# Optimization experiments

Hardware: AMD Instinct MI355X
Metric: run time of the kernel (lower is better)

## Reference

```python
import jax, jax.numpy as jnp
import numpy as np
from jax import lax

EMB, HDIM, OBS_LEN = 64, 64, 8
BATCH, NSCENES, SCENE = 32768, 4096, 8
SEQ_LEN = 12


def setup_inputs() -> dict:
    key = jax.random.key(0)
    ks = jax.random.split(key, 16)
    obs_traj = jax.random.normal(ks[0], (OBS_LEN, BATCH, 2), jnp.float32)
    last_pos = jax.random.normal(ks[1], (BATCH, 2), jnp.float32)
    last_pos_rel = jax.random.normal(ks[2], (BATCH, 2), jnp.float32)
    starts = jnp.arange(NSCENES, dtype=jnp.int32) * SCENE
    seq_start_end = jnp.stack([starts, starts + SCENE], axis=1)  # (NSCENES, 2)
    # spatial_embedding: Linear(2, EMB)
    W_se = jax.random.normal(ks[3], (EMB, 2), jnp.float32) * 0.5
    b_se = jax.random.normal(ks[4], (EMB,), jnp.float32) * 0.1
    # weight-normed convs: w = g * v / ||v||_(in,k) per out-channel, bias init zero
    def conv_params(k, cout, cin, ksz):
        ka, kb = jax.random.split(k)
        std = np.sqrt(4.0 / (ksz * cin))
        v = jax.random.normal(ka, (cout, cin, ksz), jnp.float32) * std
        g = jax.random.uniform(kb, (cout,), jnp.float32, 0.5, 1.5)
        b = jnp.zeros((cout,), jnp.float32)
        return v, g, b
    v1, g1, b1 = conv_params(ks[5], HDIM, EMB, 3)
    v2, g2, b2 = conv_params(ks[6], HDIM // 2, HDIM, 3)
    v3, g3, b3 = conv_params(ks[7], HDIM // 2, HDIM // 2, 3)
    # hidden2pos: Linear(2*HDIM, 2)
    W_hp = jax.random.normal(ks[8], (2, 2 * HDIM), jnp.float32) * 0.05
    b_hp = jax.random.normal(ks[9], (2,), jnp.float32) * 0.05
    return {"obs_traj": obs_traj, "last_pos": last_pos, "last_pos_rel": last_pos_rel,
            "W_se": W_se, "b_se": b_se,
            "v1": v1, "g1": g1, "b1": b1,
            "v2": v2, "g2": g2, "b2": b2,
            "v3": v3, "g3": g3, "b3": b3,
            "W_hp": W_hp, "b_hp": b_hp,
            "seq_start_end": seq_start_end, "seq_len": SEQ_LEN}


def _wn_conv_relu(x, v, g, b):
    # weight-norm: w[o] = g[o] * v[o] / ||v[o]||  (norm over in-channels and kernel)
    norm = jnp.sqrt(jnp.sum(v * v, axis=(1, 2)))
    w = v * (g / norm)[:, None, None]
    y = lax.conv_general_dilated(x, w, (1,), 'VALID',
                                 dimension_numbers=('NCH', 'OIH', 'NCH'))
    return jax.nn.relu(y + b[None, :, None])


def reference(obs_traj, last_pos, last_pos_rel,
              W_se, b_se, v1, g1, b1, v2, g2, b2, v3, g3, b3, W_hp, b_hp,
              seq_start_end, seq_len):
    batch = last_pos.shape[0]
    nseg = seq_start_end.shape[0]
    h_dim = v1.shape[0]
    # scene id for each pedestrian (segments are contiguous [start,end) ranges)
    seg = jnp.searchsorted(seq_start_end[:, 0], jnp.arange(batch), side='right') - 1
    # obs_traj embedding -> (batch, EMB, OBS_LEN)
    emb = obs_traj @ W_se.T + b_se            # (T, B, EMB)
    obs_emb0 = jnp.transpose(emb, (1, 2, 0))  # (B, EMB, T)

    def step(carry, _):
        obs_emb, lp = carry
        s = _wn_conv_relu(obs_emb, v1, g1, b1)   # (B, H, T-2)
        s = _wn_conv_relu(s, v2, g2, b2)         # (B, H/2, T-4)
        s = _wn_conv_relu(s, v3, g3, b3)         # (B, H/2, T-6)
        s = s.reshape(batch, h_dim)              # (H/2)*(T-6) == H
        mx = jax.ops.segment_max(s, seg, num_segments=nseg)  # ragged per-scene max
        st = jnp.concatenate([s, mx[seg]], axis=1)           # (B, 2H)
        rel = st @ W_hp.T + b_hp                 # (B, 2)
        lp = rel + lp
        dec = rel @ W_se.T + b_se                # (B, EMB)
        obs_emb = jnp.concatenate([obs_emb[:, :, 1:], dec[:, :, None]], axis=2)
        return (obs_emb, lp), rel

    _, rels = lax.scan(step, (obs_emb0, last_pos), None, length=seq_len)
    return rels  # (seq_len, batch, 2)
```

## Files before the change

### kernel.cpp

```cpp
#include <hip/hip_runtime.h>

#define BATCH 32768
#define SEQLEN 12
#define PEDS 16
#define NBLK (BATCH/PEDS)

typedef short short8 __attribute__((ext_vector_type(8)));
typedef float f32x4 __attribute__((ext_vector_type(4)));

static __device__ __forceinline__ unsigned short f2bf(float x) {
    unsigned u = __float_as_uint(x);
    return (unsigned short)((u + 0x7FFFu + ((u >> 16) & 1u)) >> 16);
}
static __device__ __forceinline__ float bf2f(unsigned short h) {
    return __uint_as_float(((unsigned)h) << 16);
}
static __device__ __forceinline__ int mod6(int h) {
    h = (h >= 12) ? h - 12 : h;
    return (h >= 6) ? h - 6 : h;
}

__global__ __launch_bounds__(256, 3)
void enc_main(const float* __restrict__ obs,
              const float* __restrict__ Wse, const float* __restrict__ bse,
              const float* __restrict__ v1, const float* __restrict__ g1, const float* __restrict__ b1,
              const float* __restrict__ v2, const float* __restrict__ g2, const float* __restrict__ b2,
              const float* __restrict__ v3, const float* __restrict__ g3, const float* __restrict__ b3,
              const float* __restrict__ Whp, const float* __restrict__ bhp,
              float* __restrict__ out)
{
    __shared__ __align__(16) float pos[8][PEDS][2];
    __shared__ __align__(16) unsigned short s1h[6][PEDS][72], s1l[6][PEDS][72];
    __shared__ __align__(16) unsigned short s2h[4][PEDS][40], s2l[4][PEDS][40];
    __shared__ __align__(16) float sff[2][PEDS][68];
    __shared__ __align__(16) float mxs[2][2][68];

    float* wse_s = &sff[0][0][0];
    float* bse_s = wse_s + 128;
    float* sc_s  = wse_s + 192;
    float* a1c   = wse_s + 320;
    float* b1c   = wse_s + 512;
    float* c1c   = wse_s + 704;

    const int tid  = threadIdx.x;
    const int wv   = tid >> 6;
    const int lane = tid & 63;
    const int n    = lane & 15;
    const int kg   = lane >> 4;

    if (tid < 128) wse_s[tid] = Wse[tid];
    else if (tid < 192) bse_s[tid-128] = bse[tid-128];
    if (tid < 64) {
        const float* v = v1 + tid*192; float s = 0.f;
        for (int j = 0; j < 192; j++) s += v[j]*v[j];
        sc_s[tid] = g1[tid] / sqrtf(s);
    } else if (tid < 96) {
        const float* v = v2 + (tid-64)*192; float s = 0.f;
        for (int j = 0; j < 192; j++) s += v[j]*v[j];
        sc_s[tid] = g2[tid-64] / sqrtf(s);
    } else if (tid < 128) {
        const float* v = v3 + (tid-96)*96; float s = 0.f;
        for (int j = 0; j < 96; j++) s += v[j]*v[j];
        sc_s[tid] = g3[tid-96] / sqrtf(s);
    }
    __syncthreads();

    {
        int tau = tid >> 5, p = (tid >> 1) & 15, c = tid & 1;
        pos[tau][p][c] = obs[(tau*BATCH + blockIdx.x*PEDS + p)*2 + c];
    }
    if (tid < 192) {
        int oc = tid & 63, tap = tid >> 6;
        const float* vr = v1 + oc*192 + tap;
        float dA = 0.f, dB = 0.f, dC = 0.f;
        #pragma unroll 8
        for (int ic = 0; ic < 64; ++ic) {
            float w = vr[ic*3];
            dA = fmaf(w, wse_s[ic*2],   dA);
            dB = fmaf(w, wse_s[ic*2+1], dB);
            dC = fmaf(w, bse_s[ic],     dC);
        }
        a1c[tap*64+oc] = dA; b1c[tap*64+oc] = dB; c1c[tap*64+oc] = dC;
    }
    __syncthreads();

    const int c_p = tid >> 4, c_oc0 = (tid & 15) * 4;
    float cA[3][4], cB[3][4], K1[4];
    #pragma unroll
    for (int j = 0; j < 4; ++j) {
        int oc = c_oc0 + j; float s = sc_s[oc];
        float cs = 0.f;
        #pragma unroll
        for (int tap = 0; tap < 3; ++tap) {
            cA[tap][j] = s * a1c[tap*64+oc];
            cB[tap][j] = s * b1c[tap*64+oc];
            cs += c1c[tap*64+oc];
        }
        K1[j] = fmaf(s, cs, b1[oc]);
    }
    short8 wBh[6], wBl[6];
    float  bBr[4];
    if (wv < 2) {
        int oc = wv*16 + n; float s = sc_s[64 + oc];
        #pragma unroll
        for (int kb = 0; kb < 6; ++kb) {
            int tap = kb >> 1, ich = kb & 1;
            #pragma unroll
            for (int j = 0; j < 8; ++j) {
                int ic = ich*32 + kg*8 + j;
                float w = v2[(oc*64 + ic)*3 + tap] * s;
                unsigned short hb = f2bf(w);
                wBh[kb][j] = (short)hb;
                wBl[kb][j] = (short)f2bf(w - bf2f(hb));
            }
        }
        #pragma unroll
        for (int r = 0; r < 4; ++r) bBr[r] = b2[wv*16 + kg*4 + r];
    } else {
        int oc = (wv-2)*16 + n; float s = sc_s[96 + oc];
        #pragma unroll
        for (int kb = 0; kb < 3; ++kb) {
            #pragma unroll
            for (int j = 0; j < 8; ++j) {
                int ic = kg*8 + j;
                float w = v3[(oc*32 + ic)*3 + kb] * s;
                unsigned short hb = f2bf(w);
                wBh[kb][j] = (short)hb;
                wBl[kb][j] = (short)f2bf(w - bf2f(hb));
            }
        }
        #pragma unroll
        for (int r = 0; r < 4; ++r) bBr[r] = b3[(wv-2)*16 + kg*4 + r];
    }
    const int e_p = tid >> 4, e_d = (tid >> 3) & 1, e_sl = tid & 7;
    float wreg[16];
    #pragma unroll
    for (int j = 0; j < 16; ++j) wreg[j] = Whp[e_d*128 + e_sl*16 + j];
    const float bhps = bhp[e_d];

    for (int t = 0; t < 6; ++t) {
        float2 pa = *(const float2*)&pos[t  ][c_p][0];
        float2 pb = *(const float2*)&pos[t+1][c_p][0];
        float2 pc = *(const float2*)&pos[t+2][c_p][0];
        unsigned hw[2], lw[2];
        #pragma unroll
        for (int q = 0; q < 2; ++q) {
            float va, vb;
            {
                int j = q*2;
                va = K1[j];
                va = fmaf(cA[0][j], pa.x, va); va = fmaf(cB[0][j], pa.y, va);
                va = fmaf(cA[1][j], pb.x, va); va = fmaf(cB[1][j], pb.y, va);
                va = fmaf(cA[2][j], pc.x, va); va = fmaf(cB[2][j], pc.y, va);
                va = fmaxf(va, 0.f);
            }
            {
                int j = q*2+1;
                vb = K1[j];
                vb = fmaf(cA[0][j], pa.x, vb); vb = fmaf(cB[0][j], pa.y, vb);
                vb = fmaf(cA[1][j], pb.x, vb); vb = fmaf(cB[1][j], pb.y, vb);
                vb = fmaf(cA[2][j], pc.x, vb); vb = fmaf(cB[2][j], pc.y, vb);
                vb = fmaxf(vb, 0.f);
            }
            unsigned short ha = f2bf(va), hb = f2bf(vb);
            hw[q] = (unsigned)ha | ((unsigned)hb << 16);
            lw[q] = (unsigned)f2bf(va - bf2f(ha)) | ((unsigned)f2bf(vb - bf2f(hb)) << 16);
        }
        *(uint2*)&s1h[t][c_p][c_oc0] = make_uint2(hw[0], hw[1]);
        *(uint2*)&s1l[t][c_p][c_oc0] = make_uint2(lw[0], lw[1]);
    }
    __syncthreads();

    for (int st = 0; st < SEQLEN; ++st) {
        if (wv < 2) {
            for (int t = (st ? 3 : 0); t < 4; ++t) {
                f32x4 a1 = {0.f,0.f,0.f,0.f}, a2 = {0.f,0.f,0.f,0.f}, a3 = {0.f,0.f,0.f,0.f};
                #pragma unroll
                for (int kb = 0; kb < 6; ++kb) {
                    int slot = mod6(st + t + (kb >> 1));
                    int off  = (kb & 1)*32 + kg*8;
                    short8 bh = *(const short8*)&s1h[slot][n][off];
                    short8 bl = *(const short8*)&s1l[slot][n][off];
                    a1 = __builtin_amdgcn_mfma_f32_16x16x32_bf16(wBh[kb], bh, a1, 0, 0, 0);
                    a2 = __builtin_amdgcn_mfma_f32_16x16x32_bf16(wBh[kb], bl, a2, 0, 0, 0);
                    a3 = __builtin_amdgcn_mfma_f32_16x16x32_bf16(wBl[kb], bh, a3, 0, 0, 0);
                }
                int slot2 = (st + t) & 3, oc0 = wv*16 + kg*4;
                float v0 = fmaxf(a1[0]+a2[0]+a3[0]+bBr[0], 0.f);
                float v1_ = fmaxf(a1[1]+a2[1]+a3[1]+bBr[1], 0.f);
                float v2_ = fmaxf(a1[2]+a2[2]+a3[2]+bBr[2], 0.f);
                float v3_ = fmaxf(a1[3]+a2[3]+a3[3]+bBr[3], 0.f);
                unsigned short h0=f2bf(v0), h1=f2bf(v1_), h2=f2bf(v2_), h3=f2bf(v3_);
                *(uint2*)&s2h[slot2][n][oc0] = make_uint2(
                    (unsigned)h0 | ((unsigned)h1 << 16), (unsigned)h2 | ((unsigned)h3 << 16));
                *(uint2*)&s2l[slot2][n][oc0] = make_uint2(
                    (unsigned)f2bf(v0-bf2f(h0)) | ((unsigned)f2bf(v1_-bf2f(h1)) << 16),
                    (unsigned)f2bf(v2_-bf2f(h2)) | ((unsigned)f2bf(v3_-bf2f(h3)) << 16));
            }
        }
        __syncthreads();

        if (wv >= 2) {
            for (int t = (st ? 1 : 0); t < 2; ++t) {
                f32x4 a1 = {0.f,0.f,0.f,0.f}, a2 = {0.f,0.f,0.f,0.f}, a3 = {0.f,0.f,0.f,0.f};
                #pragma unroll
                for (int kb = 0; kb < 3; ++kb) {
                    int slot = (st + t + kb) & 3;
                    short8 bh = *(const short8*)&s2h[slot][n][kg*8];
                    short8 bl = *(const short8*)&s2l[slot][n][kg*8];
                    a1 = __builtin_amdgcn_mfma_f32_16x16x32_bf16(wBh[kb], bh, a1, 0, 0, 0);
                    a2 = __builtin_amdgcn_mfma_f32_16x16x32_bf16(wBh[kb], bl, a2, 0, 0, 0);
                    a3 = __builtin_amdgcn_mfma_f32_16x16x32_bf16(wBl[kb], bh, a3, 0, 0, 0);
                }
                int sl01 = (st + t) & 1, oc0 = (wv-2)*16 + kg*4;
                float m0 = fmaxf(a1[0]+a2[0]+a3[0]+bBr[0], 0.f);
                float m1 = fmaxf(a1[1]+a2[1]+a3[1]+bBr[1], 0.f);
                float m2 = fmaxf(a1[2]+a2[2]+a3[2]+bBr[2], 0.f);
                float m3 = fmaxf(a1[3]+a2[3]+a3[3]+bBr[3], 0.f);
                *(float4*)&sff[sl01][n][oc0] = make_float4(m0, m1, m2, m3);
                #pragma unroll
                for (int msk = 1; msk <= 4; msk <<= 1) {
                    m0 = fmaxf(m0, __shfl_xor(m0, msk));
                    m1 = fmaxf(m1, __shfl_xor(m1, msk));
                    m2 = fmaxf(m2, __shfl_xor(m2, msk));
                    m3 = fmaxf(m3, __shfl_xor(m3, msk));
                }
                if ((n & 7) == 0)
                    *(float4*)&mxs[sl01][n >> 3][oc0] = make_float4(m0, m1, m2, m3);
            }
        }
        __syncthreads();

        {
            int sE = st & 1, sO = (st + 1) & 1;
            float pv;
            if (e_sl < 4) {
                const float* A = &sff[sE][e_p][e_sl*8];
                const float* B = &sff[sO][e_p][e_sl*8];
                float4 a0 = *(const float4*)A, aq = *(const float4*)(A+4);
                float4 b0 = *(const float4*)B, bq = *(const float4*)(B+4);
                pv = wreg[0]*a0.x + wreg[1]*b0.x + wreg[2]*a0.y + wreg[3]*b0.y
                   + wreg[4]*a0.z + wreg[5]*b0.z + wreg[6]*a0.w + wreg[7]*b0.w
                   + wreg[8]*aq.x + wreg[9]*bq.x + wreg[10]*aq.y + wreg[11]*bq.y
                   + wreg[12]*aq.z + wreg[13]*bq.z + wreg[14]*aq.w + wreg[15]*bq.w;
            } else {
                int scn = e_p >> 3;
                const float* A = &mxs[sE][scn][(e_sl-4)*8];
                const float* B = &mxs[sO][scn][(e_sl-4)*8];
                float4 a0 = *(const float4*)A, aq = *(const float4*)(A+4);
                float4 b0 = *(const float4*)B, bq = *(const float4*)(B+4);
                pv = wreg[0]*a0.x + wreg[1]*b0.x + wreg[2]*a0.y + wreg[3]*b0.y
                   + wreg[4]*a0.z + wreg[5]*b0.z + wreg[6]*a0.w + wreg[7]*b0.w
                   + wreg[8]*aq.x + wreg[9]*bq.x + wreg[10]*aq.y + wreg[11]*bq.y
                   + wreg[12]*aq.z + wreg[13]*bq.z + wreg[14]*aq.w + wreg[15]*bq.w;
            }
            pv += __shfl_xor(pv, 1);
            pv += __shfl_xor(pv, 2);
            pv += __shfl_xor(pv, 4);
            float rm = pv + bhps;
            float ro = __shfl_xor(rm, 8);
            float r0 = e_d ? ro : rm;
            float r1 = e_d ? rm : ro;
            if (e_sl == 0)
                out[(st*BATCH + blockIdx.x*PEDS + e_p)*2 + e_d] = rm;
            if (st < SEQLEN-1) {
                float2 pa = *(const float2*)&pos[(st+6)&7][e_p][0];
                float2 pb = *(const float2*)&pos[(st+7)&7][e_p][0];
                int slot5 = mod6(st + 6);
                unsigned hw[2], lw[2];
                #pragma unroll
                for (int q = 0; q < 2; ++q) {
                    float va, vb;
                    {
                        int j = q*2;
                        va = K1[j];
                        va = fmaf(cA[0][j], pa.x, va); va = fmaf(cB[0][j], pa.y, va);
                        va = fmaf(cA[1][j], pb.x, va); va = fmaf(cB[1][j], pb.y, va);
                        va = fmaf(cA[2][j], r0,   va); va = fmaf(cB[2][j], r1,   va);
                        va = fmaxf(va, 0.f);
                    }
                    {
                        int j = q*2+1;
                        vb = K1[j];
                        vb = fmaf(cA[0][j], pa.x, vb); vb = fmaf(cB[0][j], pa.y, vb);
                        vb = fmaf(cA[1][j], pb.x, vb); vb = fmaf(cB[1][j], pb.y, vb);
                        vb = fmaf(cA[2][j], r0,   vb); vb = fmaf(cB[2][j], r1,   vb);
                        vb = fmaxf(vb, 0.f);
                    }
                    unsigned short ha = f2bf(va), hb = f2bf(vb);
                    hw[q] = (unsigned)ha | ((unsigned)hb << 16);
                    lw[q] = (unsigned)f2bf(va - bf2f(ha)) | ((unsigned)f2bf(vb - bf2f(hb)) << 16);
                }
                *(uint2*)&s1h[slot5][c_p][c_oc0] = make_uint2(hw[0], hw[1]);
                *(uint2*)&s1l[slot5][c_p][c_oc0] = make_uint2(lw[0], lw[1]);
                if (e_sl == 0)
                    pos[st & 7][e_p][e_d] = rm;
            }
        }
        __syncthreads();
    }
}

extern "C" void kernel_launch(void* const* d_in, const int* in_sizes, int n_in,
                              void* d_out, int out_size, void* d_ws, size_t ws_size,
                              hipStream_t stream)
{
    const float* obs = (const float*)d_in[0];
    const float* Wse = (const float*)d_in[3];
    const float* bse = (const float*)d_in[4];
    const float* v1  = (const float*)d_in[5];
    const float* g1  = (const float*)d_in[6];
    const float* b1  = (const float*)d_in[7];
    const float* v2  = (const float*)d_in[8];
    const float* g2  = (const float*)d_in[9];
    const float* b2  = (const float*)d_in[10];
    const float* v3  = (const float*)d_in[11];
    const float* g3  = (const float*)d_in[12];
    const float* b3  = (const float*)d_in[13];
    const float* Whp = (const float*)d_in[14];
    const float* bhp = (const float*)d_in[15];

    enc_main<<<NBLK, 256, 0, stream>>>(obs, Wse, bse, v1, g1, b1, v2, g2, b2,
                                       v3, g3, b3, Whp, bhp, (float*)d_out);
}
```

Measured before the change: 209.4 us.

## Restructure conv pipeline into per-column stages with 4-slot ring buffers

New measurement: 261.2 us. 24.7% more time.

```diff
diff --git a/kernel.cpp b/kernel.cpp
--- a/kernel.cpp
+++ b/kernel.cpp
@@ -15,12 +15,8 @@
 static __device__ __forceinline__ float bf2f(unsigned short h) {
     return __uint_as_float(((unsigned)h) << 16);
 }
-static __device__ __forceinline__ int mod6(int h) {
-    h = (h >= 12) ? h - 12 : h;
-    return (h >= 6) ? h - 6 : h;
-}
-
-__global__ __launch_bounds__(256, 3)
+
+__global__ __launch_bounds__(256, 4)
 void enc_main(const float* __restrict__ obs,
               const float* __restrict__ Wse, const float* __restrict__ bse,
               const float* __restrict__ v1, const float* __restrict__ g1, const float* __restrict__ b1,
@@ -30,7 +26,7 @@
               float* __restrict__ out)
 {
     __shared__ __align__(16) float pos[8][PEDS][2];
-    __shared__ __align__(16) unsigned short s1h[6][PEDS][72], s1l[6][PEDS][72];
+    __shared__ __align__(16) unsigned short s1h[4][PEDS][72], s1l[4][PEDS][72];
     __shared__ __align__(16) unsigned short s2h[4][PEDS][40], s2l[4][PEDS][40];
     __shared__ __align__(16) float sff[2][PEDS][68];
     __shared__ __align__(16) float mxs[2][2][68];
@@ -41,7 +37,6 @@
     float* a1c   = wse_s + 320;
     float* b1c   = wse_s + 512;
     float* c1c   = wse_s + 704;
-
     const int tid  = threadIdx.x;
     const int wv   = tid >> 6;
     const int lane = tid & 63;
@@ -132,16 +127,13 @@
         #pragma unroll
         for (int r = 0; r < 4; ++r) bBr[r] = b3[(wv-2)*16 + kg*4 + r];
     }
-    const int e_p = tid >> 4, e_d = (tid >> 3) & 1, e_sl = tid & 7;
+    const int e_d = (tid >> 3) & 1, e_sl = tid & 7;
     float wreg[16];
     #pragma unroll
     for (int j = 0; j < 16; ++j) wreg[j] = Whp[e_d*128 + e_sl*16 + j];
     const float bhps = bhp[e_d];
 
-    for (int t = 0; t < 6; ++t) {
-        float2 pa = *(const float2*)&pos[t  ][c_p][0];
-        float2 pb = *(const float2*)&pos[t+1][c_p][0];
-        float2 pc = *(const float2*)&pos[t+2][c_p][0];
+    auto conv1_write = [&](int slot, float2 pa, float2 pb, float cx, float cy) {
         unsigned hw[2], lw[2];
         #pragma unroll
         for (int q = 0; q < 2; ++q) {
@@ -151,7 +143,7 @@
                 va = K1[j];
                 va = fmaf(cA[0][j], pa.x, va); va = fmaf(cB[0][j], pa.y, va);
                 va = fmaf(cA[1][j], pb.x, va); va = fmaf(cB[1][j], pb.y, va);
-                va = fmaf(cA[2][j], pc.x, va); va = fmaf(cB[2][j], pc.y, va);
+                va = fmaf(cA[2][j], cx,   va); va = fmaf(cB[2][j], cy,   va);
                 va = fmaxf(va, 0.f);
             }
             {
@@ -159,84 +151,92 @@
                 vb = K1[j];
                 vb = fmaf(cA[0][j], pa.x, vb); vb = fmaf(cB[0][j], pa.y, vb);
                 vb = fmaf(cA[1][j], pb.x, vb); vb = fmaf(cB[1][j], pb.y, vb);
-                vb = fmaf(cA[2][j], pc.x, vb); vb = fmaf(cB[2][j], pc.y, vb);
+                vb = fmaf(cA[2][j], cx,   vb); vb = fmaf(cB[2][j], cy,   vb);
                 vb = fmaxf(vb, 0.f);
             }
             unsigned short ha = f2bf(va), hb = f2bf(vb);
             hw[q] = (unsigned)ha | ((unsigned)hb << 16);
             lw[q] = (unsigned)f2bf(va - bf2f(ha)) | ((unsigned)f2bf(vb - bf2f(hb)) << 16);
         }
-        *(uint2*)&s1h[t][c_p][c_oc0] = make_uint2(hw[0], hw[1]);
-        *(uint2*)&s1l[t][c_p][c_oc0] = make_uint2(lw[0], lw[1]);
-    }
+        *(uint2*)&s1h[slot][c_p][c_oc0] = make_uint2(hw[0], hw[1]);
+        *(uint2*)&s1l[slot][c_p][c_oc0] = make_uint2(lw[0], lw[1]);
+    };
+    auto conv1_obs_col = [&](int c) {
+        float2 pa = *(const float2*)&pos[c  ][c_p][0];
+        float2 pb = *(const float2*)&pos[c+1][c_p][0];
+        float2 pc = *(const float2*)&pos[c+2][c_p][0];
+        conv1_write(c & 3, pa, pb, pc.x, pc.y);
+    };
+    auto conv2_col = [&](int c) {
+        f32x4 a1 = {0.f,0.f,0.f,0.f}, a2 = {0.f,0.f,0.f,0.f}, a3 = {0.f,0.f,0.f,0.f};
+        #pragma unroll
+        for (int kb = 0; kb < 6; ++kb) {
+            int slot = (c + (kb >> 1)) & 3;
+            int off  = (kb & 1)*32 + kg*8;
+            short8 bh = *(const short8*)&s1h[slot][n][off];
+            short8 bl = *(const short8*)&s1l[slot][n][off];
+            a1 = __builtin_amdgcn_mfma_f32_16x16x32_bf16(wBh[kb], bh, a1, 0, 0, 0);
+            a2 = __builtin_amdgcn_mfma_f32_16x16x32_bf16(wBh[kb], bl, a2, 0, 0, 0);
+            a3 = __builtin_amdgcn_mfma_f32_16x16x32_bf16(wBl[kb], bh, a3, 0, 0, 0);
+        }
+        int slot2 = c & 3, oc0 = wv*16 + kg*4;
+        float v0  = fmaxf(a1[0]+a2[0]+a3[0]+bBr[0], 0.f);
+        float v1_ = fmaxf(a1[1]+a2[1]+a3[1]+bBr[1], 0.f);
+        float v2_ = fmaxf(a1[2]+a2[2]+a3[2]+bBr[2], 0.f);
+        float v3_ = fmaxf(a1[3]+a2[3]+a3[3]+bBr[3], 0.f);
+        unsigned short h0=f2bf(v0), h1=f2bf(v1_), h2=f2bf(v2_), h3=f2bf(v3_);
+        *(uint2*)&s2h[slot2][n][oc0] = make_uint2(
+            (unsigned)h0 | ((unsigned)h1 << 16), (unsigned)h2 | ((unsigned)h3 << 16));
+        *(uint2*)&s2l[slot2][n][oc0] = make_uint2(
+            (unsigned)f2bf(v0-bf2f(h0)) | ((unsigned)f2bf(v1_-bf2f(h1)) << 16),
+            (unsigned)f2bf(v2_-bf2f(h2)) | ((unsigned)f2bf(v3_-bf2f(h3)) << 16));
+    };
+    auto conv3_col = [&](int v) {
+        f32x4 a1 = {0.f,0.f,0.f,0.f}, a2 = {0.f,0.f,0.f,0.f}, a3 = {0.f,0.f,0.f,0.f};
+        #pragma unroll
+        for (int kb = 0; kb < 3; ++kb) {
+            int slot = (v + kb) & 3;
+            short8 bh = *(const short8*)&s2h[slot][n][kg*8];
+            short8 bl = *(const short8*)&s2l[slot][n][kg*8];
+            a1 = __builtin_amdgcn_mfma_f32_16x16x32_bf16(wBh[kb], bh, a1, 0, 0, 0);
+            a2 = __builtin_amdgcn_mfma_f32_16x16x32_bf16(wBh[kb], bl, a2, 0, 0, 0);
+            a3 = __builtin_amdgcn_mfma_f32_16x16x32_bf16(wBl[kb], bh, a3, 0, 0, 0);
+        }
+        int sl01 = v & 1, oc0 = (wv-2)*16 + kg*4;
+        float m0 = fmaxf(a1[0]+a2[0]+a3[0]+bBr[0], 0.f);
+        float m1 = fmaxf(a1[1]+a2[1]+a3[1]+bBr[1], 0.f);
+        float m2 = fmaxf(a1[2]+a2[2]+a3[2]+bBr[2], 0.f);
+        float m3 = fmaxf(a1[3]+a2[3]+a3[3]+bBr[3], 0.f);
+        *(float4*)&sff[sl01][n][oc0] = make_float4(m0, m1, m2, m3);
+        #pragma unroll
+        for (int msk = 1; msk <= 4; msk <<= 1) {
+            m0 = fmaxf(m0, __shfl_xor(m0, msk));
+            m1 = fmaxf(m1, __shfl_xor(m1, msk));
+            m2 = fmaxf(m2, __shfl_xor(m2, msk));
+            m3 = fmaxf(m3, __shfl_xor(m3, msk));
+        }
+        if ((n & 7) == 0)
+            *(float4*)&mxs[sl01][n >> 3][oc0] = make_float4(m0, m1, m2, m3);
+    };
+
+    conv1_obs_col(0); conv1_obs_col(1); conv1_obs_col(2); conv1_obs_col(3);
+    __syncthreads();
+    if (wv < 2) { conv2_col(0); conv2_col(1); }
+    __syncthreads();
+    conv1_obs_col(4); conv1_obs_col(5);
+    __syncthreads();
+    if (wv < 2) { conv2_col(2); conv2_col(3); }
+    __syncthreads();
+    if (wv >= 2) { conv3_col(0); conv3_col(1); }
     __syncthreads();
 
     for (int st = 0; st < SEQLEN; ++st) {
-        if (wv < 2) {
-            for (int t = (st ? 3 : 0); t < 4; ++t) {
-                f32x4 a1 = {0.f,0.f,0.f,0.f}, a2 = {0.f,0.f,0.f,0.f}, a3 = {0.f,0.f,0.f,0.f};
-                #pragma unroll
-                for (int kb = 0; kb < 6; ++kb) {
-                    int slot = mod6(st + t + (kb >> 1));
-                    int off  = (kb & 1)*32 + kg*8;
-                    short8 bh = *(const short8*)&s1h[slot][n][off];
-                    short8 bl = *(const short8*)&s1l[slot][n][off];
-                    a1 = __builtin_amdgcn_mfma_f32_16x16x32_bf16(wBh[kb], bh, a1, 0, 0, 0);
-                    a2 = __builtin_amdgcn_mfma_f32_16x16x32_bf16(wBh[kb], bl, a2, 0, 0, 0);
-                    a3 = __builtin_amdgcn_mfma_f32_16x16x32_bf16(wBl[kb], bh, a3, 0, 0, 0);
-                }
-                int slot2 = (st + t) & 3, oc0 = wv*16 + kg*4;
-                float v0 = fmaxf(a1[0]+a2[0]+a3[0]+bBr[0], 0.f);
-                float v1_ = fmaxf(a1[1]+a2[1]+a3[1]+bBr[1], 0.f);
-                float v2_ = fmaxf(a1[2]+a2[2]+a3[2]+bBr[2], 0.f);
-                float v3_ = fmaxf(a1[3]+a2[3]+a3[3]+bBr[3], 0.f);
-                unsigned short h0=f2bf(v0), h1=f2bf(v1_), h2=f2bf(v2_), h3=f2bf(v3_);
-                *(uint2*)&s2h[slot2][n][oc0] = make_uint2(
-                    (unsigned)h0 | ((unsigned)h1 << 16), (unsigned)h2 | ((unsigned)h3 << 16));
-                *(uint2*)&s2l[slot2][n][oc0] = make_uint2(
-                    (unsigned)f2bf(v0-bf2f(h0)) | ((unsigned)f2bf(v1_-bf2f(h1)) << 16),
-                    (unsigned)f2bf(v2_-bf2f(h2)) | ((unsigned)f2bf(v3_-bf2f(h3)) << 16));
-            }
-        }
-        __syncthreads();
-
-        if (wv >= 2) {
-            for (int t = (st ? 1 : 0); t < 2; ++t) {
-                f32x4 a1 = {0.f,0.f,0.f,0.f}, a2 = {0.f,0.f,0.f,0.f}, a3 = {0.f,0.f,0.f,0.f};
-                #pragma unroll
-                for (int kb = 0; kb < 3; ++kb) {
-                    int slot = (st + t + kb) & 3;
-                    short8 bh = *(const short8*)&s2h[slot][n][kg*8];
-                    short8 bl = *(const short8*)&s2l[slot][n][kg*8];
-                    a1 = __builtin_amdgcn_mfma_f32_16x16x32_bf16(wBh[kb], bh, a1, 0, 0, 0);
-                    a2 = __builtin_amdgcn_mfma_f32_16x16x32_bf16(wBh[kb], bl, a2, 0, 0, 0);
-                    a3 = __builtin_amdgcn_mfma_f32_16x16x32_bf16(wBl[kb], bh, a3, 0, 0, 0);
-                }
-                int sl01 = (st + t) & 1, oc0 = (wv-2)*16 + kg*4;
-                float m0 = fmaxf(a1[0]+a2[0]+a3[0]+bBr[0], 0.f);
-                float m1 = fmaxf(a1[1]+a2[1]+a3[1]+bBr[1], 0.f);
-                float m2 = fmaxf(a1[2]+a2[2]+a3[2]+bBr[2], 0.f);
-                float m3 = fmaxf(a1[3]+a2[3]+a3[3]+bBr[3], 0.f);
-                *(float4*)&sff[sl01][n][oc0] = make_float4(m0, m1, m2, m3);
-                #pragma unroll
-                for (int msk = 1; msk <= 4; msk <<= 1) {
-                    m0 = fmaxf(m0, __shfl_xor(m0, msk));
-                    m1 = fmaxf(m1, __shfl_xor(m1, msk));
-                    m2 = fmaxf(m2, __shfl_xor(m2, msk));
-                    m3 = fmaxf(m3, __shfl_xor(m3, msk));
-                }
-                if ((n & 7) == 0)
-                    *(float4*)&mxs[sl01][n >> 3][oc0] = make_float4(m0, m1, m2, m3);
-            }
-        }
-        __syncthreads();
-
         {
             int sE = st & 1, sO = (st + 1) & 1;
             float pv;
             if (e_sl < 4) {
-                const float* A = &sff[sE][e_p][e_sl*8];
-                const float* B = &sff[sO][e_p][e_sl*8];
+                const float* A = &sff[sE][c_p][e_sl*8];
+                const float* B = &sff[sO][c_p][e_sl*8];
                 float4 a0 = *(const float4*)A, aq = *(const float4*)(A+4);
                 float4 b0 = *(const float4*)B, bq = *(const float4*)(B+4);
                 pv = wreg[0]*a0.x + wreg[1]*b0.x + wreg[2]*a0.y + wreg[3]*b0.y
@@ -244,7 +244,7 @@
                    + wreg[8]*aq.x + wreg[9]*bq.x + wreg[10]*aq.y + wreg[11]*bq.y
                    + wreg[12]*aq.z + wreg[13]*bq.z + wreg[14]*aq.w + wreg[15]*bq.w;
             } else {
-                int scn = e_p >> 3;
+                int scn = c_p >> 3;
                 const float* A = &mxs[sE][scn][(e_sl-4)*8];
                 const float* B = &mxs[sO][scn][(e_sl-4)*8];
                 float4 a0 = *(const float4*)A, aq = *(const float4*)(A+4);
@@ -262,41 +262,20 @@
             float r0 = e_d ? ro : rm;
             float r1 = e_d ? rm : ro;
             if (e_sl == 0)
-                out[(st*BATCH + blockIdx.x*PEDS + e_p)*2 + e_d] = rm;
+                out[(st*BATCH + blockIdx.x*PEDS + c_p)*2 + e_d] = rm;
             if (st < SEQLEN-1) {
-                float2 pa = *(const float2*)&pos[(st+6)&7][e_p][0];
-                float2 pb = *(const float2*)&pos[(st+7)&7][e_p][0];
-                int slot5 = mod6(st + 6);
-                unsigned hw[2], lw[2];
-                #pragma unroll
-                for (int q = 0; q < 2; ++q) {
-                    float va, vb;
-                    {
-                        int j = q*2;
-                        va = K1[j];
-                        va = fmaf(cA[0][j], pa.x, va); va = fmaf(cB[0][j], pa.y, va);
-                        va = fmaf(cA[1][j], pb.x, va); va = fmaf(cB[1][j], pb.y, va);
-                        va = fmaf(cA[2][j], r0,   va); va = fmaf(cB[2][j], r1,   va);
-                        va = fmaxf(va, 0.f);
-                    }
-                    {
-                        int j = q*2+1;
-                        vb = K1[j];
-                        vb = fmaf(cA[0][j], pa.x, vb); vb = fmaf(cB[0][j], pa.y, vb);
-                        vb = fmaf(cA[1][j], pb.x, vb); vb = fmaf(cB[1][j], pb.y, vb);
-                        vb = fmaf(cA[2][j], r0,   vb); vb = fmaf(cB[2][j], r1,   vb);
-                        vb = fmaxf(vb, 0.f);
-                    }
-                    unsigned short ha = f2bf(va), hb = f2bf(vb);
-                    hw[q] = (unsigned)ha | ((unsigned)hb << 16);
-                    lw[q] = (unsigned)f2bf(va - bf2f(ha)) | ((unsigned)f2bf(vb - bf2f(hb)) << 16);
-                }
-                *(uint2*)&s1h[slot5][c_p][c_oc0] = make_uint2(hw[0], hw[1]);
-                *(uint2*)&s1l[slot5][c_p][c_oc0] = make_uint2(lw[0], lw[1]);
+                float2 pa = *(const float2*)&pos[(st+6)&7][c_p][0];
+                float2 pb = *(const float2*)&pos[(st+7)&7][c_p][0];
+                conv1_write((st+6)&3, pa, pb, r0, r1);
                 if (e_sl == 0)
-                    pos[st & 7][e_p][e_d] = rm;
-            }
-        }
+                    pos[st & 7][c_p][e_d] = rm;
+            }
+        }
+        if (st == SEQLEN-1) break;
+        __syncthreads();
+        if (wv < 2) conv2_col(st + 4);
+        __syncthreads();
+        if (wv >= 2) conv3_col(st + 2);
         __syncthreads();
     }
 }
```
